# Kernel tuning notes

Measured on AMD Instinct MI355X. Metric: run time of the kernel, lower is better.

The kernel has to match this reference:

```python
import jax, jax.numpy as jnp
import numpy as np

B, N, D = 8, 4096, 256
T = 768          # text_dim
E = 4            # num_experts
K = 2            # top_k
GS = 64          # grid_size = img_size // patch_size
WS = 8           # swin window size
NH = 4           # swin heads
MODES = 16       # fno modes
HID = 4 * D      # mlp hidden


def setup_inputs() -> dict:
    key = jax.random.key(0)
    ks = jax.random.split(key, 40)
    rn = lambda k, s, sc=0.02: jax.random.normal(k, s, jnp.float32) * sc
    return {
        "x": jax.random.normal(ks[0], (B, N, D), jnp.float32),
        "text_embedding": jax.random.normal(ks[1], (B, T), jnp.float32),
        # TopKGating: Linear(D+T->D), ReLU, Linear(D->E)
        "g1_w": rn(ks[2], (D, D + T)), "g1_b": jnp.zeros((D,), jnp.float32),
        "g2_w": rn(ks[3], (E, D)), "g2_b": jnp.zeros((E,), jnp.float32),
        # FNOExpert: SpectralConv2d complex weights (real/imag) + 1x1 conv
        "fno_w1r": rn(ks[4], (D, D, MODES, MODES), 1.0 / D), "fno_w1i": rn(ks[5], (D, D, MODES, MODES), 1.0 / D),
        "fno_w2r": rn(ks[6], (D, D, MODES, MODES), 1.0 / D), "fno_w2i": rn(ks[7], (D, D, MODES, MODES), 1.0 / D),
        "fno_cw": rn(ks[8], (D, D)), "fno_cb": jnp.zeros((D,), jnp.float32),
        # MLPExpert #1
        "m1_w1": rn(ks[9], (HID, D)), "m1_b1": jnp.zeros((HID,), jnp.float32),
        "m1_w2": rn(ks[10], (D, HID)), "m1_b2": jnp.zeros((D,), jnp.float32),
        # WindowAttentionExpert
        "a_ln1w": jnp.ones((D,), jnp.float32), "a_ln1b": jnp.zeros((D,), jnp.float32),
        "a_qkvw": rn(ks[11], (3 * D, D)), "a_qkvb": jnp.zeros((3 * D,), jnp.float32),
        "a_ow": rn(ks[12], (D, D)), "a_ob": jnp.zeros((D,), jnp.float32),
        "a_ln2w": jnp.ones((D,), jnp.float32), "a_ln2b": jnp.zeros((D,), jnp.float32),
        "a_mw1": rn(ks[13], (HID, D)), "a_mb1": jnp.zeros((HID,), jnp.float32),
        "a_mw2": rn(ks[14], (D, HID)), "a_mb2": jnp.zeros((D,), jnp.float32),
        # MLPExpert #2 (extra expert to reach num_experts=4)
        "m2_w1": rn(ks[15], (HID, D)), "m2_b1": jnp.zeros((HID,), jnp.float32),
        "m2_w2": rn(ks[16], (D, HID)), "m2_b2": jnp.zeros((D,), jnp.float32),
    }


def _gelu(v):
    return jax.nn.gelu(v, approximate=False)


def _ln(v, g, b, eps=1e-5):
    m = v.mean(-1, keepdims=True)
    var = ((v - m) ** 2).mean(-1, keepdims=True)
    return (v - m) * jax.lax.rsqrt(var + eps) * g + b


def reference(x, text_embedding, g1_w, g1_b, g2_w, g2_b,
              fno_w1r, fno_w1i, fno_w2r, fno_w2i, fno_cw, fno_cb,
              m1_w1, m1_b1, m1_w2, m1_b2,
              a_ln1w, a_ln1b, a_qkvw, a_qkvb, a_ow, a_ob,
              a_ln2w, a_ln2b, a_mw1, a_mb1, a_mw2, a_mb2,
              m2_w1, m2_b1, m2_w2, m2_b2):
    Bb, Nn, Dd = x.shape

    # ---- TopKGating ----
    feat = jnp.concatenate([x.mean(axis=1), text_embedding], axis=1)   # [B, D+T]
    h = jax.nn.relu(feat @ g1_w.T + g1_b)
    logits = h @ g2_w.T + g2_b                                         # [B, E]
    vals, idx = jax.lax.top_k(logits, K)
    w = jax.nn.softmax(vals, axis=1)                                   # [B, K]
    # per-(sample, expert) combine weight; indices are constants
    combine = (w[..., None] * jax.nn.one_hot(idx, E, dtype=x.dtype)).sum(axis=1)  # [B, E]

    # ---- Expert 0: FNO ----
    def fno(v):
        xg = v.transpose(0, 2, 1).reshape(Bb, Dd, GS, GS)              # [B, D, H, W]
        xft = jnp.fft.rfft2(xg)                                        # [B, D, H, W//2+1]
        w1 = fno_w1r + 1j * fno_w1i
        w2 = fno_w2r + 1j * fno_w2i
        lo = jnp.einsum('bixy,ioxy->boxy', xft[:, :, :MODES, :MODES], w1)
        hi = jnp.einsum('bixy,ioxy->boxy', xft[:, :, -MODES:, :MODES], w2)
        out_ft = jnp.zeros_like(xft)
        out_ft = out_ft.at[:, :, :MODES, :MODES].set(lo)
        out_ft = out_ft.at[:, :, -MODES:, :MODES].set(hi)
        x1 = jnp.fft.irfft2(out_ft, s=(GS, GS))
        x2 = jnp.einsum('bihw,oi->bohw', xg, fno_cw) + fno_cb[None, :, None, None]
        out = _gelu(x1 + x2)
        return out.reshape(Bb, Dd, Nn).transpose(0, 2, 1) + v

    # ---- MLP experts ----
    def mlp(v, w1, b1, w2, b2):
        return _gelu(v @ w1.T + b1) @ w2.T + b2 + v

    # ---- Expert 2: window attention ----
    def win_attn(v):
        xs = _ln(v, a_ln1w, a_ln1b).reshape(Bb, GS, GS, Dd)
        nw = GS // WS
        xw = xs.reshape(Bb, nw, WS, nw, WS, Dd).transpose(0, 1, 3, 2, 4, 5)
        xw = xw.reshape(-1, WS * WS, Dd)                               # [B*nw*nw, L, D]
        qkv = xw @ a_qkvw.T + a_qkvb
        q, k, vv = jnp.split(qkv, 3, axis=-1)
        dh = Dd // NH
        heads = lambda t: t.reshape(-1, WS * WS, NH, dh).transpose(0, 2, 1, 3)
        q, k, vv = heads(q), heads(k), heads(vv)
        attn = jax.nn.softmax(q @ k.transpose(0, 1, 3, 2) / jnp.sqrt(jnp.float32(dh)), axis=-1)
        o = (attn @ vv).transpose(0, 2, 1, 3).reshape(-1, WS * WS, Dd) @ a_ow.T + a_ob
        o = o.reshape(Bb, nw, nw, WS, WS, Dd).transpose(0, 1, 3, 2, 4, 5).reshape(Bb, Nn, Dd)
        v2 = v + o
        return v2 + (_gelu(_ln(v2, a_ln2w, a_ln2b) @ a_mw1.T + a_mb1) @ a_mw2.T + a_mb2)

    outs = [fno(x),
            mlp(x, m1_w1, m1_b1, m1_w2, m1_b2),
            win_attn(x),
            mlp(x, m2_w1, m2_b1, m2_w2, m2_b2)]
    final = sum(combine[:, e, None, None] * outs[e] for e in range(E))
    return final, w
```

## Files before the change

kernel.cpp:

```cpp
#include <hip/hip_runtime.h>
#include <math.h>

#define BB 8
#define NN 4096
#define DDIM 256
#define TT 768
#define BND (BB*NN*DDIM)

typedef unsigned short ushort_t;
typedef short bf16x8 __attribute__((ext_vector_type(8)));
typedef float f32x4 __attribute__((ext_vector_type(4)));

__device__ __forceinline__ float gelu_f(float v){
    return 0.5f * v * (1.0f + erff(v * 0.70710678118654752f));
}
__device__ __forceinline__ ushort_t f2bf(float f){
    union { float f; unsigned int u; } v; v.f = f;
    unsigned int u = v.u;
    u += 0x7FFFu + ((u >> 16) & 1u);
    return (ushort_t)(u >> 16);
}
__device__ __forceinline__ float bf2f(ushort_t h){
    union { unsigned int u; float f; } v; v.u = ((unsigned int)h) << 16;
    return v.f;
}
__device__ __forceinline__ float pk_re(unsigned int p){
    union { unsigned int u; float f; } v; v.u = p << 16; return v.f;
}
__device__ __forceinline__ float pk_im(unsigned int p){
    union { unsigned int u; float f; } v; v.u = p & 0xffff0000u; return v.f;
}
#define GLOAD16(gp, lp) __builtin_amdgcn_global_load_lds( \
    (__attribute__((address_space(1))) const void*)(gp),  \
    (__attribute__((address_space(3))) void*)(lp), 16, 0, 0)

__global__ __launch_bounds__(256) void k_meanA(const float* __restrict__ x, float* __restrict__ partial){
    int c = blockIdx.x, b = blockIdx.y, t = threadIdx.x;
    const float* p = x + ((size_t)b*NN + c*256)*DDIM + t;
    float s0=0,s1=0,s2=0,s3=0;
    for (int n=0;n<256;n+=4){
        s0 += p[(size_t)n*DDIM];
        s1 += p[(size_t)(n+1)*DDIM];
        s2 += p[(size_t)(n+2)*DDIM];
        s3 += p[(size_t)(n+3)*DDIM];
    }
    partial[((size_t)b*16 + c)*256 + t] = (s0+s1)+(s2+s3);
}

__global__ __launch_bounds__(256) void k_gate1(const float* __restrict__ partial, const float* __restrict__ text,
    const float* __restrict__ g1w, const float* __restrict__ g1b, float* __restrict__ hs){
    int d = blockIdx.x, t = threadIdx.x;
    int w = t >> 6, lane = t & 63;
    float xm[BB];
    #pragma unroll
    for (int b=0;b<BB;++b){
        float s = 0.f;
        #pragma unroll
        for (int c=0;c<16;++c) s += partial[((size_t)b*16 + c)*256 + t];
        xm[b] = s * (1.0f/NN);
    }
    const float* wrow = g1w + (size_t)d*(DDIM+TT);
    float w0 = wrow[t], w1 = wrow[256+t], w2 = wrow[512+t], w3 = wrow[768+t];
    float acc[BB];
    #pragma unroll
    for (int b=0;b<BB;++b){
        const float* tx = text + (size_t)b*TT;
        acc[b] = xm[b]*w0 + tx[t]*w1 + tx[256+t]*w2 + tx[512+t]*w3;
    }
    #pragma unroll
    for (int b=0;b<BB;++b)
        for (int off=32; off; off>>=1) acc[b] += __shfl_down(acc[b], off);
    __shared__ float red[BB][4];
    if (lane==0)
        #pragma unroll
        for (int b=0;b<BB;++b) red[b][w] = acc[b];
    __syncthreads();
    if (t < BB){
        float s = red[t][0]+red[t][1]+red[t][2]+red[t][3] + g1b[d];
        hs[t*DDIM + d] = fmaxf(s, 0.0f);
    }
}

__global__ __launch_bounds__(64) void k_gate2(const float* __restrict__ hs,
    const float* __restrict__ g2w, const float* __restrict__ g2b,
    float* __restrict__ combine, float* __restrict__ wout){
    __shared__ float lg[BB][4];
    int t = threadIdx.x;
    if (t < 32){
        int b = t>>2, e = t&3;
        float a = g2b[e];
        const float* w2 = g2w + e*DDIM;
        const float* h = hs + b*DDIM;
        for (int o=0;o<DDIM;o+=4)
            a += h[o]*w2[o] + h[o+1]*w2[o+1] + h[o+2]*w2[o+2] + h[o+3]*w2[o+3];
        lg[b][e] = a;
    }
    __syncthreads();
    if (t < BB){
        int b = t;
        int i1=0; float v1=lg[b][0];
        for (int e=1;e<4;++e){ if (lg[b][e] > v1){ v1=lg[b][e]; i1=e; } }
        int i2=0; float v2=-3.0e38f; bool found=false;
        for (int e=0;e<4;++e){ if (e==i1) continue; if (!found || lg[b][e] > v2){ v2=lg[b][e]; i2=e; found=true; } }
        float e2 = expf(v2 - v1);
        float inv = 1.0f/(1.0f + e2);
        float w0 = inv, w1 = e2*inv;
        float cv[4] = {0.f,0.f,0.f,0.f};
        cv[i1] = w0; cv[i2] = w1;
        for (int e=0;e<4;++e) combine[b*4+e] = cv[e];
        wout[b*2+0] = w0; wout[b*2+1] = w1;
    }
}

__global__ __launch_bounds__(256) void k_rowstats(const float* __restrict__ src, float* __restrict__ stats,
    const float* __restrict__ combine, int expert){
    int row0 = blockIdx.x*4;
    int b = row0 >> 12;
    if (expert >= 0 && combine[b*4+expert]==0.0f) return;
    int row = row0 + (threadIdx.x>>6);
    int lane = threadIdx.x & 63;
    const float* p = src + (size_t)row*DDIM;
    float s=0.f, s2=0.f;
    for (int j=lane;j<DDIM;j+=64){ float v=p[j]; s+=v; s2+=v*v; }
    for (int off=32; off; off>>=1){ s += __shfl_down(s, off); s2 += __shfl_down(s2, off); }
    if (lane==0){
        float m = s*(1.0f/DDIM);
        float var = s2*(1.0f/DDIM) - m*m;
        stats[row*2] = m;
        stats[row*2+1] = rsqrtf(var + 1e-5f);
    }
}

__global__ __launch_bounds__(256) void k_cvtw(
    const float* __restrict__ s0, const float* __restrict__ s1, const float* __restrict__ s2,
    const float* __restrict__ s3, const float* __restrict__ s4, const float* __restrict__ s5,
    const float* __restrict__ s6, const float* __restrict__ s7, const float* __restrict__ s8,
    ushort_t* __restrict__ dst){
    const int off[10] = {0,196608,262144,524288,786432,1048576,1310720,1572864,1835008,1900544};
    const float* srcs[9] = {s0,s1,s2,s3,s4,s5,s6,s7,s8};
    int i = (blockIdx.x*256 + threadIdx.x)*8;
    if (i >= 1900544) return;
    int seg = 0;
    #pragma unroll
    for (int k=1;k<9;++k) if (i >= off[k]) seg = k;
    const float* s = srcs[seg] + (i - off[seg]);
    ushort_t* d = dst + i;
    #pragma unroll
    for (int u=0;u<8;++u) d[u] = f2bf(s[u]);
}

__global__ __launch_bounds__(256) void k_xcvt(const float4* __restrict__ x, const float* __restrict__ stats,
    const float* __restrict__ lng, const float* __restrict__ lnb,
    ushort_t* __restrict__ xbf, ushort_t* __restrict__ xlnbf, float4* __restrict__ outp){
    int i4 = blockIdx.x*256 + threadIdx.x;
    int row = i4 >> 6, c0 = (i4 & 63)*4;
    float4 v = x[i4];
    outp[i4] = v;
    float m = stats[row*2], r = stats[row*2+1];
    float vv[4] = {v.x, v.y, v.z, v.w};
    #pragma unroll
    for (int u=0;u<4;++u){
        int i = i4*4 + u;
        xbf[i] = f2bf(vv[u]);
        xlnbf[i] = f2bf((vv[u]-m)*r*lng[c0+u] + lnb[c0+u]);
    }
}

__global__ __launch_bounds__(256) void k_v2cvt(const float4* __restrict__ v2, const float* __restrict__ stats,
    const float* __restrict__ lng, const float* __restrict__ lnb,
    ushort_t* __restrict__ dstbf, const float* __restrict__ combine){
    int i4 = blockIdx.x*256 + threadIdx.x;
    int row = i4 >> 6;
    if (combine[(row>>12)*4+2]==0.0f) return;
    int c0 = (i4 & 63)*4;
    float4 v = v2[i4];
    float m = stats[row*2], r = stats[row*2+1];
    float vv[4] = {v.x, v.y, v.z, v.w};
    #pragma unroll
    for (int u=0;u<4;++u)
        dstbf[i4*4+u] = f2bf((vv[u]-m)*r*lng[c0+u] + lnb[c0+u]);
}

__global__ __launch_bounds__(256) void k_transpose(const float* __restrict__ x, float* __restrict__ xT,
                                                   const float* __restrict__ combine){
    int b = blockIdx.z;
    if (combine[b*4+0]==0.0f) return;
    __shared__ float tile[32][33];
    int n0 = blockIdx.x*32, d0 = blockIdx.y*32;
    int tx = threadIdx.x, ty = threadIdx.y;
    for (int j=0;j<32;j+=8)
        tile[ty+j][tx] = x[((size_t)b*NN + n0+ty+j)*DDIM + d0+tx];
    __syncthreads();
    for (int j=0;j<32;j+=8)
        xT[((size_t)b*DDIM + d0+ty+j)*NN + n0+tx] = tile[tx][ty+j];
}

__global__ __launch_bounds__(256) void k_fft_w(const float* __restrict__ xT, float* __restrict__ F1,
                                               const float* __restrict__ combine){
    int bd = blockIdx.x; int b = bd >> 8;
    if (combine[b*4+0]==0.0f) return;
    __shared__ float img[4096];
    __shared__ float ct[64], st[64];
    int t = threadIdx.x;
    if (t < 64){ float ang = (float)t * 0.09817477042468103f; ct[t]=cosf(ang); st[t]=sinf(ang); }
    const float* src = xT + (size_t)bd*4096;
    for (int i=t;i<4096;i+=256) img[i]=src[i];
    __syncthreads();
    for (int task=t; task<1024; task+=256){
        int h = task>>4, ky = task&15;
        const float* row = img + h*64;
        float re=0.f, im=0.f;
        #pragma unroll
        for (int w=0;w<64;++w){
            int m = (ky*w)&63;
            float v = row[w];
            re += v*ct[m]; im -= v*st[m];
        }
        float2* o = (float2*)(F1 + ((size_t)bd*1024 + task)*2);
        *o = make_float2(re, im);
    }
}

__global__ __launch_bounds__(256) void k_fft_h(const float* __restrict__ F1,
                                               unsigned int* __restrict__ F2pk,
                                               const float* __restrict__ combine){
    int bd = blockIdx.x; int b = bd>>8;
    if (combine[b*4+0]==0.0f) return;
    __shared__ float f1[2048];
    __shared__ float ct[64], st[64];
    int t = threadIdx.x;
    if (t < 64){ float ang = (float)t * 0.09817477042468103f; ct[t]=cosf(ang); st[t]=sinf(ang); }
    const float* src = F1 + (size_t)bd*2048;
    for (int i=t;i<2048;i+=256) f1[i]=src[i];
    __syncthreads();
    for (int task=t; task<512; task+=256){
        int c = task>>8, kxp = (task>>4)&15, ky = task&15;
        int kx = c ? 48+kxp : kxp;
        float re=0.f, im=0.f;
        #pragma unroll
        for (int h=0;h<64;++h){
            int m = (kx*h)&63;
            float ar = f1[(h*16+ky)*2], ai = f1[(h*16+ky)*2+1];
            re += ar*ct[m] + ai*st[m];
            im += ai*ct[m] - ar*st[m];
        }
        F2pk[(size_t)bd*512 + task] = (((unsigned int)f2bf(im)) << 16) | (unsigned int)f2bf(re);
    }
}

__global__ __launch_bounds__(256) void k_specmul4(const unsigned int* __restrict__ F2pk,
    const float* __restrict__ w1r, const float* __restrict__ w1i,
    const float* __restrict__ w2r, const float* __restrict__ w2i,
    float* __restrict__ Gp, const float* __restrict__ combine){
    bool any=false;
    for (int b=0;b<BB;++b) any = any || (combine[b*4]!=0.0f);
    if (!any) return;
    int t  = threadIdx.x;
    int o0 = blockIdx.x * 2;
    int c  = blockIdx.y;
    int s  = blockIdx.z;
    const float* Wr = c ? w2r : w1r;
    const float* Wi = c ? w2i : w1i;
    float ar[2][BB], ai[2][BB];
    #pragma unroll
    for (int oo=0;oo<2;++oo)
        #pragma unroll
        for (int b=0;b<BB;++b){ ar[oo][b]=0.f; ai[oo][b]=0.f; }
    int i0 = s*32;
    for (int ii=i0; ii<i0+32; ii+=2){
        float wr[2][2], wi[2][2];
        #pragma unroll
        for (int u=0;u<2;++u)
            #pragma unroll
            for (int oo=0;oo<2;++oo){
                size_t widx = ((size_t)(ii+u)*DDIM + o0+oo)*256 + t;
                wr[u][oo] = Wr[widx];
                wi[u][oo] = Wi[widx];
            }
        unsigned int f[2][BB];
        #pragma unroll
        for (int u=0;u<2;++u)
            #pragma unroll
            for (int b=0;b<BB;++b)
                f[u][b] = F2pk[(size_t)b*131072 + (size_t)(ii+u)*512 + c*256 + t];
        #pragma unroll
        for (int u=0;u<2;++u)
            #pragma unroll
            for (int oo=0;oo<2;++oo)
                #pragma unroll
                for (int b=0;b<BB;++b){
                    float fr = pk_re(f[u][b]);
                    float fi = pk_im(f[u][b]);
                    ar[oo][b] += fr*wr[u][oo] - fi*wi[u][oo];
                    ai[oo][b] += fr*wi[u][oo] + fi*wr[u][oo];
                }
    }
    #pragma unroll
    for (int oo=0;oo<2;++oo)
        for (int b=0;b<BB;++b){
            float2* g = (float2*)(Gp + ((((size_t)s*BB + b)*DDIM + o0+oo)*512 + c*256 + t)*2);
            *g = make_float2(ar[oo][b], ai[oo][b]);
        }
}

__global__ __launch_bounds__(256) void k_ifft_h(const float* __restrict__ Gp, float* __restrict__ Z,
                                                const float* __restrict__ combine){
    int bd = blockIdx.x; int b = bd>>8;
    if (combine[b*4+0]==0.0f) return;
    __shared__ float g[1024];
    __shared__ float ct[64], st[64];
    int t=threadIdx.x;
    if (t < 64){ float ang = (float)t * 0.09817477042468103f; ct[t]=cosf(ang); st[t]=sinf(ang); }
    {
        f32x4 v = (f32x4){0.f,0.f,0.f,0.f};
        #pragma unroll
        for (int s=0;s<8;++s){
            const f32x4* p = (const f32x4*)(Gp + (size_t)s*2097152 + (size_t)bd*1024);
            v += p[t];
        }
        *(f32x4*)(g + t*4) = v;
    }
    __syncthreads();
    for (int task=t;task<1024;task+=256){
        int h=task>>4, ky=task&15;
        float re=0.f, im=0.f;
        #pragma unroll
        for (int c=0;c<2;++c){
            #pragma unroll
            for (int kxp=0;kxp<16;++kxp){
                int kx = c ? 48+kxp : kxp;
                int m = (kx*h)&63;
                int gi = (c*256 + kxp*16 + ky)*2;
                float gr=g[gi], gim=g[gi+1];
                re += gr*ct[m] - gim*st[m];
                im += gr*st[m] + gim*ct[m];
            }
        }
        float2* o = (float2*)(Z + ((size_t)bd*1024 + task)*2);
        *o = make_float2(re*(1.0f/64.0f), im*(1.0f/64.0f));
    }
}

__global__ __launch_bounds__(256) void k_fno_out(const float* __restrict__ Z, const float* __restrict__ X2,
    const float* __restrict__ combine, float* __restrict__ out){
    int h = blockIdx.x, b = blockIdx.y;
    float cb = combine[b*4];
    if (cb==0.0f) return;
    __shared__ float ct[64], st[64];
    int t = threadIdx.x;
    if (t < 64){ float ang = (float)t * 0.09817477042468103f; ct[t]=cosf(ang); st[t]=sinf(ang); }
    __syncthreads();
    float zr[16], zi[16];
    const float* zp = Z + (((size_t)(b*DDIM + t)*64 + h)*16)*2;
    #pragma unroll
    for (int ky=0;ky<16;++ky){
        float2 v = *(const float2*)(zp + ky*2);
        zr[ky]=v.x; zi[ky]=v.y;
    }
    for (int w=0;w<64;++w){
        float s = zr[0];
        #pragma unroll
        for (int ky=1;ky<16;++ky){
            int m = (ky*w)&63;
            s += 2.0f*(zr[ky]*ct[m] - zi[ky]*st[m]);
        }
        s *= (1.0f/64.0f);
        size_t idx = ((size_t)b*NN + h*64 + w)*DDIM + t;
        out[idx] += cb * gelu_f(s + X2[idx]);
    }
}

template<int EPI>
__global__ __launch_bounds__(256) void k_bgemm(
    const ushort_t* __restrict__ A, const ushort_t* __restrict__ W, const float* __restrict__ bias,
    void* __restrict__ dst, const float* __restrict__ combine, int expert, int K, int N,
    const float* __restrict__ xres, float* __restrict__ out)
{
    int tiles_n = N >> 7;
    int tm = blockIdx.x / tiles_n, tn = blockIdx.x - tm*tiles_n;
    int row0 = tm << 7, col0 = tn << 7;
    float scale = combine[(row0>>12)*4 + expert];
    if (scale == 0.0f) return;
    __shared__ __align__(16) ushort_t As[8192];
    __shared__ __align__(16) ushort_t Bs[8192];
    int t = threadIdx.x;
    int w = t >> 6, lane = t & 63;
    int wr = w >> 1, wc = w & 1;
    int lrow = lane >> 3, lk8 = (lane & 7) * 8;
    f32x4 acc[4][4];
    #pragma unroll
    for (int m=0;m<4;++m)
        #pragma unroll
        for (int n=0;n<4;++n) acc[m][n] = (f32x4){0.f,0.f,0.f,0.f};
    int afr = lane & 15, akr = (lane >> 4) * 8;
    for (int k0=0; k0<K; k0+=64){
        #pragma unroll
        for (int it=0; it<4; ++it){
            int c = it*4 + w;
            const ushort_t* ga = A + (size_t)(row0 + c*8 + lrow)*K + k0 + lk8;
            GLOAD16(ga, As + c*512);
            const ushort_t* gb = W + (size_t)(col0 + c*8 + lrow)*K + k0 + lk8;
            GLOAD16(gb, Bs + c*512);
        }
        __syncthreads();
        #pragma unroll
        for (int kk=0; kk<2; ++kk){
            bf16x8 af[4], bfr[4];
            #pragma unroll
            for (int m=0;m<4;++m)
                af[m] = *(const bf16x8*)(As + (wr*64 + m*16 + afr)*64 + kk*32 + akr);
            #pragma unroll
            for (int n=0;n<4;++n)
                bfr[n] = *(const bf16x8*)(Bs + (wc*64 + n*16 + afr)*64 + kk*32 + akr);
            #pragma unroll
            for (int m=0;m<4;++m)
                #pragma unroll
                for (int n=0;n<4;++n)
                    acc[m][n] = __builtin_amdgcn_mfma_f32_16x16x32_bf16(af[m], bfr[n], acc[m][n], 0, 0, 0);
        }
        __syncthreads();
    }
    int rbase = row0 + wr*64 + (lane>>4)*4;
    int cbase = col0 + wc*64 + (lane&15);
    #pragma unroll
    for (int n=0;n<4;++n){
        int col = cbase + n*16;
        float bcol = bias[col];
        #pragma unroll
        for (int m=0;m<4;++m){
            int r0 = rbase + m*16;
            f32x4 a = acc[m][n];
            #pragma unroll
            for (int j=0;j<4;++j){
                int r = r0 + j;
                float v = a[j] + bcol;
                if (EPI==0)      ((ushort_t*)dst)[(size_t)r*N + col] = f2bf(v);
                else if (EPI==1) ((ushort_t*)dst)[(size_t)r*N + col] = f2bf(gelu_f(v));
                else if (EPI==2) out[(size_t)r*DDIM + col] += scale * v;
                else if (EPI==3){
                    ((float*)dst)[(size_t)r*DDIM + col] = xres[(size_t)r*DDIM + col] + v;
                    out[(size_t)r*DDIM + col] += scale * v;
                } else {
                    ((float*)dst)[(size_t)r*DDIM + col] = v;
                }
            }
        }
    }
}

__global__ __launch_bounds__(256) void k_attn(const ushort_t* __restrict__ QKV, ushort_t* __restrict__ O,
                                              const float* __restrict__ combine){
    int wh = blockIdx.x;
    int w = wh>>2, head = wh&3;
    int b = w>>6;
    if (combine[b*4+2]==0.0f) return;
    int i1 = (w>>3)&7, i2 = w&7;
    __shared__ float A1[64][64];
    __shared__ float kk[64][65];
    __shared__ float S[64][65];
    int t = threadIdx.x;
    for (int idx=t; idx<4096; idx+=256){
        int l = idx>>6, dc = idx&63;
        int n = b*NN + (i1*8 + (l>>3))*64 + i2*8 + (l&7);
        const ushort_t* qrow = QKV + (size_t)n*768;
        A1[l][dc] = bf2f(qrow[head*64+dc]);
        kk[l][dc] = bf2f(qrow[256+head*64+dc]);
    }
    __syncthreads();
    for (int idx=t; idx<4096; idx+=256){
        int i=idx>>6, j=idx&63;
        float s=0.f;
        #pragma unroll 8
        for (int dc=0;dc<64;++dc) s += A1[i][dc]*kk[j][dc];
        S[i][j] = s * 0.125f;
    }
    __syncthreads();
    for (int idx=t; idx<4096; idx+=256){
        int l = idx>>6, dc = idx&63;
        int n = b*NN + (i1*8 + (l>>3))*64 + i2*8 + (l&7);
        A1[l][dc] = bf2f(QKV[(size_t)n*768 + 512 + head*64 + dc]);
    }
    __syncthreads();
    if (t < 64){
        float mx = -3.0e38f;
        for (int j=0;j<64;++j) mx = fmaxf(mx, S[t][j]);
        float sum=0.f;
        for (int j=0;j<64;++j){ float e = expf(S[t][j]-mx); S[t][j]=e; sum+=e; }
        float inv = 1.0f/sum;
        for (int j=0;j<64;++j) S[t][j] *= inv;
    }
    __syncthreads();
    for (int idx=t; idx<4096; idx+=256){
        int i=idx>>6, dc=idx&63;
        float s=0.f;
        #pragma unroll 8
        for (int j=0;j<64;++j) s += S[i][j]*A1[j][dc];
        int n = b*NN + (i1*8 + (i>>3))*64 + i2*8 + (i&7);
        O[(size_t)n*DDIM + head*64 + dc] = f2bf(s);
    }
}

extern "C" void kernel_launch(void* const* d_in, const int* in_sizes, int n_in,
                              void* d_out, int out_size, void* d_ws, size_t ws_size,
                              hipStream_t stream) {
    (void)in_sizes; (void)n_in; (void)out_size; (void)ws_size;
    const float* x      = (const float*)d_in[0];
    const float* text   = (const float*)d_in[1];
    const float* g1_w   = (const float*)d_in[2];
    const float* g1_b   = (const float*)d_in[3];
    const float* g2_w   = (const float*)d_in[4];
    const float* g2_b   = (const float*)d_in[5];
    const float* w1r    = (const float*)d_in[6];
    const float* w1i    = (const float*)d_in[7];
    const float* w2r    = (const float*)d_in[8];
    const float* w2i    = (const float*)d_in[9];
    const float* fno_cw = (const float*)d_in[10];
    const float* fno_cb = (const float*)d_in[11];
    const float* m1_w1  = (const float*)d_in[12];
    const float* m1_b1  = (const float*)d_in[13];
    const float* m1_w2  = (const float*)d_in[14];
    const float* m1_b2  = (const float*)d_in[15];
    const float* a_ln1w = (const float*)d_in[16];
    const float* a_ln1b = (const float*)d_in[17];
    const float* a_qkvw = (const float*)d_in[18];
    const float* a_qkvb = (const float*)d_in[19];
    const float* a_ow   = (const float*)d_in[20];
    const float* a_ob   = (const float*)d_in[21];
    const float* a_ln2w = (const float*)d_in[22];
    const float* a_ln2b = (const float*)d_in[23];
    const float* a_mw1  = (const float*)d_in[24];
    const float* a_mb1  = (const float*)d_in[25];
    const float* a_mw2  = (const float*)d_in[26];
    const float* a_mb2  = (const float*)d_in[27];
    const float* m2_w1  = (const float*)d_in[28];
    const float* m2_b1  = (const float*)d_in[29];
    const float* m2_w2  = (const float*)d_in[30];
    const float* m2_b2  = (const float*)d_in[31];

    float* out  = (float*)d_out;
    float* wout = out + (size_t)BND;

    float* wsf     = (float*)d_ws;
    float* hs      = wsf;
    float* combine = wsf + 2048;
    float* stats   = wsf + 4096;
    ushort_t* wbf  = (ushort_t*)(wsf + 69632);
    float* partial = wsf + 1019904;
    ushort_t* x_bf   = (ushort_t*)(wsf + 1118208);
    ushort_t* xln_bf = (ushort_t*)(wsf + 5312512);
    float* R1 = wsf + 9506816;
    float* xT  = R1;
    float* Gp  = R1;
    float* F1  = R1 + 8388608;
    float* Z   = R1 + 16777216;
    float* X2  = R1 + 20971520;
    unsigned int* F2pk = (unsigned int*)(R1 + 29360128);
    ushort_t* QKV_bf  = (ushort_t*)R1;
    ushort_t* O_bf    = (ushort_t*)(R1 + 12582912);
    float*    V2      = R1 + 16777216;
    ushort_t* v2ln_bf = (ushort_t*)(R1 + 25165824);
    ushort_t* H_bf = (ushort_t*)R1;

    ushort_t* qkvw_bf = wbf + 0;
    ushort_t* ow_bf   = wbf + 196608;
    ushort_t* mw1_bf  = wbf + 262144;
    ushort_t* mw2_bf  = wbf + 524288;
    ushort_t* m1w1_bf = wbf + 786432;
    ushort_t* m1w2_bf = wbf + 1048576;
    ushort_t* m2w1_bf = wbf + 1310720;
    ushort_t* m2w2_bf = wbf + 1572864;
    ushort_t* cw_bf   = wbf + 1835008;

    k_meanA<<<dim3(16,BB), 256, 0, stream>>>(x, partial);
    k_gate1<<<256, 256, 0, stream>>>(partial, text, g1_w, g1_b, hs);
    k_gate2<<<1, 64, 0, stream>>>(hs, g2_w, g2_b, combine, wout);
    k_rowstats<<<8192, 256, 0, stream>>>(x, stats, combine, -1);
    k_cvtw<<<928, 256, 0, stream>>>(a_qkvw, a_ow, a_mw1, a_mw2, m1_w1, m1_w2, m2_w1, m2_w2, fno_cw, wbf);
    k_xcvt<<<8192, 256, 0, stream>>>((const float4*)x, stats, a_ln1w, a_ln1b, x_bf, xln_bf, (float4*)out);

    k_transpose<<<dim3(128,8,8), dim3(32,8), 0, stream>>>(x, xT, combine);
    k_fft_w<<<2048, 256, 0, stream>>>(xT, F1, combine);
    k_fft_h<<<2048, 256, 0, stream>>>(F1, F2pk, combine);
    k_specmul4<<<dim3(128,2,8), 256, 0, stream>>>(F2pk, w1r, w1i, w2r, w2i, Gp, combine);
    k_ifft_h<<<2048, 256, 0, stream>>>(Gp, Z, combine);
    k_bgemm<4><<<512, 256, 0, stream>>>(x_bf, cw_bf, fno_cb, X2, combine, 0, 256, 256, nullptr, nullptr);
    k_fno_out<<<dim3(64,8), 256, 0, stream>>>(Z, X2, combine, out);

    k_bgemm<1><<<2048, 256, 0, stream>>>(x_bf, m1w1_bf, m1_b1, H_bf, combine, 1, 256, 1024, nullptr, nullptr);
    k_bgemm<2><<<512, 256, 0, stream>>>(H_bf, m1w2_bf, m1_b2, nullptr, combine, 1, 1024, 256, nullptr, out);

    k_bgemm<0><<<1536, 256, 0, stream>>>(xln_bf, qkvw_bf, a_qkvb, QKV_bf, combine, 2, 256, 768, nullptr, nullptr);
    k_attn<<<2048, 256, 0, stream>>>(QKV_bf, O_bf, combine);
    k_bgemm<3><<<512, 256, 0, stream>>>(O_bf, ow_bf, a_ob, V2, combine, 2, 256, 256, x, out);
    k_rowstats<<<8192, 256, 0, stream>>>(V2, stats, combine, 2);
    k_v2cvt<<<8192, 256, 0, stream>>>((const float4*)V2, stats, a_ln2w, a_ln2b, v2ln_bf, combine);
    k_bgemm<1><<<2048, 256, 0, stream>>>(v2ln_bf, mw1_bf, a_mb1, H_bf, combine, 2, 256, 1024, nullptr, nullptr);
    k_bgemm<2><<<512, 256, 0, stream>>>(H_bf, mw2_bf, a_mb2, nullptr, combine, 2, 1024, 256, nullptr, out);

    k_bgemm<1><<<2048, 256, 0, stream>>>(x_bf, m2w1_bf, m2_b1, H_bf, combine, 3, 256, 1024, nullptr, nullptr);
    k_bgemm<2><<<512, 256, 0, stream>>>(H_bf, m2w2_bf, m2_b2, nullptr, combine, 3, 1024, 256, nullptr, out);
}
```

Before: 632.8 us.

## Fuse transpose into W-axis FFT, batch-interleave spectral data, store FNO conv output as bf16

The separate transpose kernel is removed. The W-direction DFT now reads 64 rows of x straight into shared memory (64 KB) and each thread computes all 16 modes for one channel. The packed spectrum is stored batch-innermost, so the spectral multiply loads all 8 batches with two 128-bit loads and uses simpler pointer strides. The FNO 1x1 conv output is kept in bf16 instead of fp32, which halves its write and read traffic but loses some precision before GELU. The larger shared-memory block and fewer blocks (512) may lower occupancy for the FFT stage.

```diff
diff --git a/kernel.cpp b/kernel.cpp
--- a/kernel.cpp
+++ b/kernel.cpp
@@ -181,50 +181,41 @@
         dstbf[i4*4+u] = f2bf((vv[u]-m)*r*lng[c0+u] + lnb[c0+u]);
 }
 
-__global__ __launch_bounds__(256) void k_transpose(const float* __restrict__ x, float* __restrict__ xT,
-                                                   const float* __restrict__ combine){
-    int b = blockIdx.z;
+__global__ __launch_bounds__(256) void k_fft_w2(const float* __restrict__ x, float* __restrict__ F1,
+                                                const float* __restrict__ combine){
+    int h = blockIdx.x, b = blockIdx.y;
     if (combine[b*4+0]==0.0f) return;
-    __shared__ float tile[32][33];
-    int n0 = blockIdx.x*32, d0 = blockIdx.y*32;
-    int tx = threadIdx.x, ty = threadIdx.y;
-    for (int j=0;j<32;j+=8)
-        tile[ty+j][tx] = x[((size_t)b*NN + n0+ty+j)*DDIM + d0+tx];
-    __syncthreads();
-    for (int j=0;j<32;j+=8)
-        xT[((size_t)b*DDIM + d0+ty+j)*NN + n0+tx] = tile[tx][ty+j];
-}
-
-__global__ __launch_bounds__(256) void k_fft_w(const float* __restrict__ xT, float* __restrict__ F1,
-                                               const float* __restrict__ combine){
-    int bd = blockIdx.x; int b = bd >> 8;
-    if (combine[b*4+0]==0.0f) return;
-    __shared__ float img[4096];
+    __shared__ float img[64*256];
     __shared__ float ct[64], st[64];
     int t = threadIdx.x;
     if (t < 64){ float ang = (float)t * 0.09817477042468103f; ct[t]=cosf(ang); st[t]=sinf(ang); }
-    const float* src = xT + (size_t)bd*4096;
-    for (int i=t;i<4096;i+=256) img[i]=src[i];
-    __syncthreads();
-    for (int task=t; task<1024; task+=256){
-        int h = task>>4, ky = task&15;
-        const float* row = img + h*64;
-        float re=0.f, im=0.f;
-        #pragma unroll
-        for (int w=0;w<64;++w){
+    {
+        const float4* src = (const float4*)(x + ((size_t)b*NN + h*64)*DDIM);
+        float4* dst4 = (float4*)img;
+        for (int i=t; i<4096; i+=256) dst4[i] = src[i];
+    }
+    __syncthreads();
+    float re[16], im[16];
+    #pragma unroll
+    for (int ky=0;ky<16;++ky){ re[ky]=0.f; im[ky]=0.f; }
+    for (int w=0; w<64; ++w){
+        float v = img[w*256 + t];
+        #pragma unroll
+        for (int ky=0; ky<16; ++ky){
             int m = (ky*w)&63;
-            float v = row[w];
-            re += v*ct[m]; im -= v*st[m];
-        }
-        float2* o = (float2*)(F1 + ((size_t)bd*1024 + task)*2);
-        *o = make_float2(re, im);
-    }
+            re[ky] += v*ct[m];
+            im[ky] -= v*st[m];
+        }
+    }
+    float2* o = (float2*)(F1 + (((size_t)(b*DDIM + t))*1024 + h*16)*2);
+    #pragma unroll
+    for (int ky=0;ky<16;++ky) o[ky] = make_float2(re[ky], im[ky]);
 }
 
 __global__ __launch_bounds__(256) void k_fft_h(const float* __restrict__ F1,
                                                unsigned int* __restrict__ F2pk,
                                                const float* __restrict__ combine){
-    int bd = blockIdx.x; int b = bd>>8;
+    int bd = blockIdx.x; int b = bd>>8, d = bd&255;
     if (combine[b*4+0]==0.0f) return;
     __shared__ float f1[2048];
     __shared__ float ct[64], st[64];
@@ -244,11 +235,11 @@
             re += ar*ct[m] + ai*st[m];
             im += ai*ct[m] - ar*st[m];
         }
-        F2pk[(size_t)bd*512 + task] = (((unsigned int)f2bf(im)) << 16) | (unsigned int)f2bf(re);
-    }
-}
-
-__global__ __launch_bounds__(256) void k_specmul4(const unsigned int* __restrict__ F2pk,
+        F2pk[((size_t)d*512 + task)*8 + b] = (((unsigned int)f2bf(im)) << 16) | (unsigned int)f2bf(re);
+    }
+}
+
+__global__ __launch_bounds__(256) void k_specmul5(const unsigned int* __restrict__ F2pk,
     const float* __restrict__ w1r, const float* __restrict__ w1i,
     const float* __restrict__ w2r, const float* __restrict__ w2i,
     float* __restrict__ Gp, const float* __restrict__ combine){
@@ -259,41 +250,31 @@
     int o0 = blockIdx.x * 2;
     int c  = blockIdx.y;
     int s  = blockIdx.z;
-    const float* Wr = c ? w2r : w1r;
-    const float* Wi = c ? w2i : w1i;
+    const float* Wr = (c ? w2r : w1r) + ((size_t)(s*32)*DDIM + o0)*256 + t;
+    const float* Wi = (c ? w2i : w1i) + ((size_t)(s*32)*DDIM + o0)*256 + t;
+    const unsigned int* Fp = F2pk + ((size_t)(s*32)*512 + c*256 + t)*8;
     float ar[2][BB], ai[2][BB];
     #pragma unroll
     for (int oo=0;oo<2;++oo)
         #pragma unroll
         for (int b=0;b<BB;++b){ ar[oo][b]=0.f; ai[oo][b]=0.f; }
-    int i0 = s*32;
-    for (int ii=i0; ii<i0+32; ii+=2){
-        float wr[2][2], wi[2][2];
-        #pragma unroll
-        for (int u=0;u<2;++u)
-            #pragma unroll
-            for (int oo=0;oo<2;++oo){
-                size_t widx = ((size_t)(ii+u)*DDIM + o0+oo)*256 + t;
-                wr[u][oo] = Wr[widx];
-                wi[u][oo] = Wi[widx];
-            }
-        unsigned int f[2][BB];
-        #pragma unroll
-        for (int u=0;u<2;++u)
-            #pragma unroll
-            for (int b=0;b<BB;++b)
-                f[u][b] = F2pk[(size_t)b*131072 + (size_t)(ii+u)*512 + c*256 + t];
-        #pragma unroll
-        for (int u=0;u<2;++u)
-            #pragma unroll
-            for (int oo=0;oo<2;++oo)
-                #pragma unroll
-                for (int b=0;b<BB;++b){
-                    float fr = pk_re(f[u][b]);
-                    float fi = pk_im(f[u][b]);
-                    ar[oo][b] += fr*wr[u][oo] - fi*wi[u][oo];
-                    ai[oo][b] += fr*wi[u][oo] + fi*wr[u][oo];
-                }
+    #pragma unroll 2
+    for (int ii=0; ii<32; ++ii){
+        float wr0 = Wr[0], wr1 = Wr[256];
+        float wi0 = Wi[0], wi1 = Wi[256];
+        uint4 fa = *(const uint4*)(Fp);
+        uint4 fb = *(const uint4*)(Fp + 4);
+        Wr += 65536; Wi += 65536; Fp += 4096;
+        unsigned int f[8] = {fa.x, fa.y, fa.z, fa.w, fb.x, fb.y, fb.z, fb.w};
+        #pragma unroll
+        for (int b=0;b<BB;++b){
+            float fr = pk_re(f[b]);
+            float fi = pk_im(f[b]);
+            ar[0][b] += fr*wr0 - fi*wi0;
+            ai[0][b] += fr*wi0 + fi*wr0;
+            ar[1][b] += fr*wr1 - fi*wi1;
+            ai[1][b] += fr*wi1 + fi*wr1;
+        }
     }
     #pragma unroll
     for (int oo=0;oo<2;++oo)
@@ -341,7 +322,7 @@
     }
 }
 
-__global__ __launch_bounds__(256) void k_fno_out(const float* __restrict__ Z, const float* __restrict__ X2,
+__global__ __launch_bounds__(256) void k_fno_out(const float* __restrict__ Z, const ushort_t* __restrict__ X2,
     const float* __restrict__ combine, float* __restrict__ out){
     int h = blockIdx.x, b = blockIdx.y;
     float cb = combine[b*4];
@@ -366,7 +347,7 @@
         }
         s *= (1.0f/64.0f);
         size_t idx = ((size_t)b*NN + h*64 + w)*DDIM + t;
-        out[idx] += cb * gelu_f(s + X2[idx]);
+        out[idx] += cb * gelu_f(s + bf2f(X2[idx]));
     }
 }
 
@@ -440,8 +421,6 @@
                 else if (EPI==3){
                     ((float*)dst)[(size_t)r*DDIM + col] = xres[(size_t)r*DDIM + col] + v;
                     out[(size_t)r*DDIM + col] += scale * v;
-                } else {
-                    ((float*)dst)[(size_t)r*DDIM + col] = v;
                 }
             }
         }
@@ -549,11 +528,10 @@
     ushort_t* x_bf   = (ushort_t*)(wsf + 1118208);
     ushort_t* xln_bf = (ushort_t*)(wsf + 5312512);
     float* R1 = wsf + 9506816;
-    float* xT  = R1;
     float* Gp  = R1;
     float* F1  = R1 + 8388608;
     float* Z   = R1 + 16777216;
-    float* X2  = R1 + 20971520;
+    ushort_t* X2_bf = (ushort_t*)(R1 + 20971520);
     unsigned int* F2pk = (unsigned int*)(R1 + 29360128);
     ushort_t* QKV_bf  = (ushort_t*)R1;
     ushort_t* O_bf    = (ushort_t*)(R1 + 12582912);
@@ -578,13 +556,12 @@
     k_cvtw<<<928, 256, 0, stream>>>(a_qkvw, a_ow, a_mw1, a_mw2, m1_w1, m1_w2, m2_w1, m2_w2, fno_cw, wbf);
     k_xcvt<<<8192, 256, 0, stream>>>((const float4*)x, stats, a_ln1w, a_ln1b, x_bf, xln_bf, (float4*)out);
 
-    k_transpose<<<dim3(128,8,8), dim3(32,8), 0, stream>>>(x, xT, combine);
-    k_fft_w<<<2048, 256, 0, stream>>>(xT, F1, combine);
+    k_fft_w2<<<dim3(64,BB), 256, 0, stream>>>(x, F1, combine);
     k_fft_h<<<2048, 256, 0, stream>>>(F1, F2pk, combine);
-    k_specmul4<<<dim3(128,2,8), 256, 0, stream>>>(F2pk, w1r, w1i, w2r, w2i, Gp, combine);
+    k_specmul5<<<dim3(128,2,8), 256, 0, stream>>>(F2pk, w1r, w1i, w2r, w2i, Gp, combine);
     k_ifft_h<<<2048, 256, 0, stream>>>(Gp, Z, combine);
-    k_bgemm<4><<<512, 256, 0, stream>>>(x_bf, cw_bf, fno_cb, X2, combine, 0, 256, 256, nullptr, nullptr);
-    k_fno_out<<<dim3(64,8), 256, 0, stream>>>(Z, X2, combine, out);
+    k_bgemm<0><<<512, 256, 0, stream>>>(x_bf, cw_bf, fno_cb, X2_bf, combine, 0, 256, 256, nullptr, nullptr);
+    k_fno_out<<<dim3(64,8), 256, 0, stream>>>(Z, X2_bf, combine, out);
 
     k_bgemm<1><<<2048, 256, 0, stream>>>(x_bf, m1w1_bf, m1_b1, H_bf, combine, 1, 256, 1024, nullptr, nullptr);
     k_bgemm<2><<<512, 256, 0, stream>>>(H_bf, m1w2_bf, m1_b2, nullptr, combine, 1, 1024, 256, nullptr, out);
```

After: 673.8 us. 1.06x slower.
